# Optimization experiments

Hardware: AMD Instinct MI355X
Metric: run time of the kernel (lower is better)

The kernel has to match this reference:

```python
import jax, jax.numpy as jnp
import numpy as np

EPS = 1e-5

def bn_eval(x, p):
    # p: [4, C] = gamma, beta, running_mean, running_var; channel-last broadcast
    g, b, m, v = p[0], p[1], p[2], p[3]
    return (x - m) * (g / jnp.sqrt(v + EPS)) + b

def _bn_params(k, c):
    k1, k2, k3, k4 = jax.random.split(k, 4)
    gamma = jax.random.uniform(k1, (c,)) + 0.5
    beta = jax.random.normal(k2, (c,)) * 0.1
    mean = jax.random.normal(k3, (c,)) * 0.1
    var = jax.random.uniform(k4, (c,)) + 0.5
    return jnp.stack([gamma, beta, mean, var])

def _lin(k, fan_in, fan_out):
    bound = 1.0 / np.sqrt(fan_in)
    kw, kb = jax.random.split(k)
    w = jax.random.uniform(kw, (fan_in, fan_out), minval=-bound, maxval=bound)
    b = jax.random.uniform(kb, (fan_out,), minval=-bound, maxval=bound)
    return w, b

def setup_inputs() -> dict:
    key = jax.random.key(0)
    B, N, S, C, G = 2, 4096, 16, 256, 8
    ks = jax.random.split(key, 20)
    feats = jax.random.normal(ks[0], (B, N, C), dtype=jnp.float32)
    coords = jax.random.normal(ks[1], (B, N, 3), dtype=jnp.float32)
    index = jax.random.randint(ks[2], (B, N, S), 0, N, dtype=jnp.int32)
    wq, bq = _lin(ks[3], C, C); bnq = _bn_params(ks[4], C)
    wk, bk = _lin(ks[5], C, C); bnk = _bn_params(ks[6], C)
    wv, bv = _lin(ks[7], C, C)
    pm_w1, pm_b1 = _lin(ks[8], 3, C); pm_bn = _bn_params(ks[9], C)
    pm_w2, pm_b2 = _lin(ks[10], C, C)
    pb_w1, pb_b1 = _lin(ks[11], 3, C); pb_bn = _bn_params(ks[12], C)
    pb_w2, pb_b2 = _lin(ks[13], C, C)
    we_w1, we_b1 = _lin(ks[14], C, G); we_bn = _bn_params(ks[15], G)
    we_w2, we_b2 = _lin(ks[16], G, G)
    return dict(feats=feats, coords=coords, index=index,
                wq=wq, bq=bq, bnq=bnq, wk=wk, bk=bk, bnk=bnk, wv=wv, bv=bv,
                pm_w1=pm_w1, pm_b1=pm_b1, pm_bn=pm_bn, pm_w2=pm_w2, pm_b2=pm_b2,
                pb_w1=pb_w1, pb_b1=pb_b1, pb_bn=pb_bn, pb_w2=pb_w2, pb_b2=pb_b2,
                we_w1=we_w1, we_b1=we_b1, we_bn=we_bn, we_w2=we_w2, we_b2=we_b2)

def reference(feats, coords, index,
              wq, bq, bnq, wk, bk, bnk, wv, bv,
              pm_w1, pm_b1, pm_bn, pm_w2, pm_b2,
              pb_w1, pb_b1, pb_bn, pb_w2, pb_b2,
              we_w1, we_b1, we_bn, we_w2, we_b2):
    B, N, C = feats.shape
    S = index.shape[2]
    G = we_w1.shape[1]
    q = jax.nn.relu(bn_eval(feats @ wq + bq, bnq))                       # [B,N,C]
    k = jax.nn.relu(bn_eval(feats @ wk + bk, bnk))                       # [B,N,C]
    v = feats @ wv + bv                                                   # [B,N,C]
    idx = index.reshape(B, N * S)
    key_g = jnp.take_along_axis(k, idx[:, :, None], axis=1).reshape(B, N, S, C)
    val_g = jnp.take_along_axis(v, idx[:, :, None], axis=1).reshape(B, N, S, C)
    crd_g = jnp.take_along_axis(coords, idx[:, :, None], axis=1).reshape(B, N, S, 3)
    relation_qk = key_g - q[:, :, None, :]                                # [B,N,S,C]
    pos = coords[:, :, None, :] - crd_g                                   # [B,N,S,3]
    pem = jax.nn.relu(bn_eval(pos @ pm_w1 + pm_b1, pm_bn)) @ pm_w2 + pm_b2
    relation_qk = relation_qk * pem
    peb = jax.nn.relu(bn_eval(pos @ pb_w1 + pb_b1, pb_bn)) @ pb_w2 + pb_b2
    relation_qk = relation_qk + peb
    val_g = val_g + peb
    w = jax.nn.relu(bn_eval(relation_qk @ we_w1 + we_b1, we_bn)) @ we_w2 + we_b2  # [B,N,S,G]
    w = jax.nn.softmax(w, axis=2)                                         # softmax over neighbors
    val_g = val_g.reshape(B, N, S, G, C // G)
    out = jnp.einsum('bnsgi,bnsg->bngi', val_g, w).reshape(B, N, C)
    return out
```

## Files before the change

### kernel.cpp

```cpp
#include <hip/hip_runtime.h>
#include <hip/hip_bf16.h>


typedef __attribute__((ext_vector_type(8))) short bf16x8_t;
typedef __attribute__((ext_vector_type(4))) float f32x4_t;
typedef __attribute__((ext_vector_type(2))) float v2f;

#define BN_EPS 1e-5f
#define WSYNC() asm volatile("s_waitcnt lgkmcnt(0)" ::: "memory")

__device__ __forceinline__ float blo(unsigned int v) {
    union { unsigned int u; float f; } x; x.u = v << 16; return x.f;
}
__device__ __forceinline__ float bhi(unsigned int v) {
    union { unsigned int u; float f; } x; x.u = v & 0xffff0000u; return x.f;
}
__device__ __forceinline__ v2f upk(unsigned int v) {
    v2f r; r.x = blo(v); r.y = bhi(v); return r;
}
__device__ __forceinline__ unsigned int fbits(float f) {
    union { float f; unsigned int u; } x; x.f = f; return x.u;
}
__device__ __forceinline__ unsigned short f2b(float f) {
    unsigned int u = fbits(f);
    return (unsigned short)((u + 0x7fffu + ((u >> 16) & 1u)) >> 16);
}
__device__ __forceinline__ unsigned int f2bpk(float a, float b) {
    union { __hip_bfloat162 h; unsigned int u; } x;
    x.h = __float22bfloat162_rn(make_float2(a, b));
    return x.u;
}
__device__ __forceinline__ unsigned int f2bpk2(v2f v) { return f2bpk(v.x, v.y); }
__device__ __forceinline__ unsigned int relpair(unsigned int kb, unsigned int qb,
                                                unsigned int pm_, unsigned int pb_) {
    v2f d = upk(kb) - upk(qb);
    v2f r = __builtin_elementwise_fma(d, upk(pm_), upk(pb_));
    return f2bpk2(r);
}

__global__ __launch_bounds__(256) void k_prep(
    const float* __restrict__ wq, const float* __restrict__ wk,
    const float* __restrict__ wv, const float* __restrict__ pm2,
    const float* __restrict__ pb2,
    const float* __restrict__ pm_w1, const float* __restrict__ pm_b1,
    const float* __restrict__ pm_bn,
    const float* __restrict__ pb_w1, const float* __restrict__ pb_b1,
    const float* __restrict__ pb_bn,
    const float* __restrict__ we_w1,
    unsigned short* __restrict__ wsT, float* __restrict__ W4,
    unsigned short* __restrict__ we1TF)
{
    const int bid = blockIdx.x, t = threadIdx.x;
    if (bid < 160) {
        __shared__ unsigned short T[32][72];
        const int mat = bid >> 5;
        const int kk  = (bid >> 2) & 7;
        const int ntq = bid & 3;
        const float* s = (mat == 0) ? wq : (mat == 1) ? wk : (mat == 2) ? wv
                         : (mat == 3) ? pm2 : pb2;
        {
            int c = t & 63, r0 = t >> 6;
            for (int i = 0; i < 8; ++i) {
                int r = r0 + i * 4;
                T[r][c] = f2b(s[(kk * 32 + r) * 256 + ntq * 64 + c]);
            }
        }
        __syncthreads();
        {
            int seg = t >> 6, lane = t & 63;
            int col = seg * 16 + (lane & 15);
            int kr  = (lane >> 4) * 8;
            unsigned int v[8];
            #pragma unroll
            for (int j = 0; j < 8; ++j) v[j] = T[kr + j][col];
            uint4 o;
            o.x = v[0] | (v[1] << 16);
            o.y = v[2] | (v[3] << 16);
            o.z = v[4] | (v[5] << 16);
            o.w = v[6] | (v[7] << 16);
            *(uint4*)(wsT + mat * 65536 + (ntq * 4 + seg) * 4096 + kk * 512 + lane * 8) = o;
        }
    } else if (bid == 160) {
        int c = t;
        float s = pm_bn[c] / sqrtf(pm_bn[768 + c] + BN_EPS);
        float4 wm = make_float4(pm_w1[c] * s, pm_w1[256 + c] * s, pm_w1[512 + c] * s,
                                (pm_b1[c] - pm_bn[512 + c]) * s + pm_bn[256 + c]);
        s = pb_bn[c] / sqrtf(pb_bn[768 + c] + BN_EPS);
        float4 wb = make_float4(pb_w1[c] * s, pb_w1[256 + c] * s, pb_w1[512 + c] * s,
                                (pb_b1[c] - pb_bn[512 + c]) * s + pb_bn[256 + c]);
        ((float4*)W4)[c]       = wm;
        ((float4*)W4)[256 + c] = wb;
    } else {
        for (int j = 0; j < 8; ++j) {
            int e = t * 8 + j;
            int g = e >> 8, c = e & 255;
            we1TF[g * 256 + c] = f2b(we_w1[c * 8 + g]);
        }
    }
}

__global__ __launch_bounds__(256) void k_qkv(
    const float* __restrict__ feats,
    const unsigned short* __restrict__ wT,
    const float* __restrict__ bq, const float* __restrict__ bnq,
    const float* __restrict__ bk, const float* __restrict__ bnk,
    const float* __restrict__ bv,
    unsigned short* __restrict__ qkv)
{
    __shared__ unsigned short A[32][264];
    const int t    = threadIdx.x;
    const int widx = blockIdx.x >> 8;
    const int mb   = blockIdx.x & 255;

    for (int i = 0; i < 8; ++i) {
        int row = 4 * i + (t >> 6), col = (t & 63) * 4;
        float4 f = *(const float4*)(feats + (mb * 32 + row) * 256 + col);
        *(uint2*)&A[row][col] = make_uint2(f2bpk(f.x, f.y), f2bpk(f.z, f.w));
    }
    __syncthreads();

    const int lane = t & 63, w = t >> 6;
    const int ln15 = lane & 15, quad = lane >> 4;
    const int mt = w & 1, nh = w >> 1;

    bf16x8_t afr[8];
    #pragma unroll
    for (int kk = 0; kk < 8; ++kk)
        afr[kk] = *(const bf16x8_t*)&A[mt * 16 + ln15][kk * 32 + quad * 8];

    const unsigned short* W = wT + widx * 65536;
    const float* bias = (widx == 0) ? bq : (widx == 1) ? bk : bv;
    const float* bn   = (widx == 0) ? bnq : (widx == 1) ? bnk : nullptr;
    unsigned short* dst = qkv + (size_t)widx * 8192 * 256;

    f32x4_t acc[8];
    for (int j = 0; j < 8; ++j) acc[j] = (f32x4_t){0.f, 0.f, 0.f, 0.f};

    #pragma unroll
    for (int kk = 0; kk < 8; ++kk) {
        #pragma unroll
        for (int j = 0; j < 8; ++j) {
            int nt = nh * 8 + j;
            bf16x8_t bfr = *(const bf16x8_t*)(W + ((nt * 8 + kk) * 64 + lane) * 8);
            acc[j] = __builtin_amdgcn_mfma_f32_16x16x32_bf16(afr[kk], bfr, acc[j], 0, 0, 0);
        }
    }

    float bb[8], sc[8], mu[8], be[8];
    #pragma unroll
    for (int j = 0; j < 8; ++j) {
        int c = (nh * 8 + j) * 16 + ln15;
        bb[j] = bias[c];
        if (bn) {
            sc[j] = bn[c] / sqrtf(bn[768 + c] + BN_EPS);
            be[j] = bn[256 + c];
            mu[j] = bn[512 + c];
        }
    }
    __syncthreads();
    #pragma unroll
    for (int j = 0; j < 8; ++j) {
        int c = (nh * 8 + j) * 16 + ln15;
        float y[4];
        for (int r = 0; r < 4; ++r) {
            y[r] = acc[j][r] + bb[j];
            if (bn) y[r] = fmaxf((y[r] - mu[j]) * sc[j] + be[j], 0.f);
        }
        for (int r = 0; r < 4; r += 2) {
            unsigned int pk = f2bpk(y[r], y[r + 1]);
            A[mt * 16 + quad * 4 + r][c]     = (unsigned short)pk;
            A[mt * 16 + quad * 4 + r + 1][c] = (unsigned short)(pk >> 16);
        }
    }
    __syncthreads();
    {
        int row = t >> 3, cc = (t & 7) * 32;
        #pragma unroll
        for (int j = 0; j < 4; ++j) {
            uint4 v = *(const uint4*)&A[row][cc + 8 * j];
            *(uint4*)(dst + (mb * 32 + row) * 256 + cc + 8 * j) = v;
        }
    }
}

__global__ __launch_bounds__(512, 4) void k_main(
    const float* __restrict__ coords,
    const int*   __restrict__ index,
    const unsigned short* __restrict__ qm,
    const unsigned short* __restrict__ km,
    const unsigned short* __restrict__ vm,
    const unsigned short* __restrict__ pmw2F,
    const unsigned short* __restrict__ pbw2F,
    const float* __restrict__ W4,
    const unsigned short* __restrict__ we1TF,
    const float* __restrict__ pm_b2, const float* __restrict__ pb_b2,
    const float* __restrict__ we_b1, const float* __restrict__ we_bn,
    const float* __restrict__ we_w2, const float* __restrict__ we_b2,
    float* __restrict__ out)
{
    __shared__ unsigned short bufR[64][264];
    __shared__ unsigned short bufP[64][264];
    __shared__ float posA[64][4];
    __shared__ float usP[2][64][8];
    __shared__ float us_[64][8];
    __shared__ int   rowg_[64];
    __shared__ float we2s[8][8];
    __shared__ float web2[8], swe8[8], dwe8[8];

    const int t   = threadIdx.x;
    const int P0  = blockIdx.x * 4;
    const int bb_ = P0 >> 12;
    const int w = t >> 6, lane = t & 63;
    const int ln15 = lane & 15, quad = lane >> 4;
    const int p   = w >> 1, sub = w & 1;
    const int R0  = p * 16;
    const int Pg  = P0 + p;

    const int rg = (bb_ << 12) + index[Pg * 16 + ln15];
    uint4 kpre[4];
    #pragma unroll
    for (int kk = 0; kk < 4; ++kk)
        kpre[kk] = *(const uint4*)(km + rg * 256 + (sub * 4 + kk) * 32 + quad * 8);

    if (lane < 8) {
        int m  = w * 8 + lane;
        int Pr = P0 + (m >> 4);
        int rs = (bb_ << 12) + index[Pr * 16 + (m & 15)];
        rowg_[m]   = rs;
        posA[m][0] = coords[Pr * 3 + 0] - coords[rs * 3 + 0];
        posA[m][1] = coords[Pr * 3 + 1] - coords[rs * 3 + 1];
        posA[m][2] = coords[Pr * 3 + 2] - coords[rs * 3 + 2];
        posA[m][3] = 0.f;
    }
    if (t < 64) we2s[t >> 3][t & 7] = we_w2[t];
    if (t < 8) {
        float s = we_bn[t] / sqrtf(we_bn[24 + t] + BN_EPS);
        swe8[t] = s;
        dwe8[t] = (we_b1[t] - we_bn[16 + t]) * s + we_bn[8 + t];
        web2[t] = we_b2[t];
    }
    WSYNC();

    const int hc = lane * 4;
    const int hm = w * 8;

    v2f w0a, w1a, w2a, w3a, w0b, w1b, w2b, w3b;
    v2f x0a, x1a, x2a, x3a, x0b, x1b, x2b, x3b;
    {
        float4 A0 = ((const float4*)W4)[hc],     A1 = ((const float4*)W4)[hc + 1];
        float4 A2 = ((const float4*)W4)[hc + 2], A3 = ((const float4*)W4)[hc + 3];
        w0a = (v2f){A0.x, A1.x}; w1a = (v2f){A0.y, A1.y};
        w2a = (v2f){A0.z, A1.z}; w3a = (v2f){A0.w, A1.w};
        w0b = (v2f){A2.x, A3.x}; w1b = (v2f){A2.y, A3.y};
        w2b = (v2f){A2.z, A3.z}; w3b = (v2f){A2.w, A3.w};
        float4 B0 = ((const float4*)W4)[256 + hc],     B1 = ((const float4*)W4)[256 + hc + 1];
        float4 B2 = ((const float4*)W4)[256 + hc + 2], B3 = ((const float4*)W4)[256 + hc + 3];
        x0a = (v2f){B0.x, B1.x}; x1a = (v2f){B0.y, B1.y};
        x2a = (v2f){B0.z, B1.z}; x3a = (v2f){B0.w, B1.w};
        x0b = (v2f){B2.x, B3.x}; x1b = (v2f){B2.y, B3.y};
        x2b = (v2f){B2.z, B3.z}; x3b = (v2f){B2.w, B3.w};
    }
    const v2f vz = {0.f, 0.f};

    #pragma unroll
    for (int m = 0; m < 8; ++m) {
        float4 pp = *(const float4*)&posA[hm + m][0];
        v2f px = (v2f){pp.x, pp.x}, py = (v2f){pp.y, pp.y}, pz = (v2f){pp.z, pp.z};
        v2f ha = __builtin_elementwise_fma(px, x0a,
                 __builtin_elementwise_fma(py, x1a,
                 __builtin_elementwise_fma(pz, x2a, x3a)));
        v2f hb = __builtin_elementwise_fma(px, x0b,
                 __builtin_elementwise_fma(py, x1b,
                 __builtin_elementwise_fma(pz, x2b, x3b)));
        ha = __builtin_elementwise_max(ha, vz);
        hb = __builtin_elementwise_max(hb, vz);
        *(uint2*)&bufR[hm + m][hc] = make_uint2(f2bpk2(ha), f2bpk2(hb));
    }
    __syncthreads();

    f32x4_t acc[2][4];
    {
        float b0 = pb_b2[(w * 2    ) * 16 + ln15];
        float b1 = pb_b2[(w * 2 + 1) * 16 + ln15];
        for (int mt = 0; mt < 4; ++mt) {
            acc[0][mt] = (f32x4_t){b0, b0, b0, b0};
            acc[1][mt] = (f32x4_t){b1, b1, b1, b1};
        }
    }
    #pragma unroll
    for (int kk = 0; kk < 8; ++kk) {
        bf16x8_t afr[4];
        #pragma unroll
        for (int mt = 0; mt < 4; ++mt)
            afr[mt] = *(const bf16x8_t*)&bufR[mt * 16 + ln15][kk * 32 + quad * 8];
        #pragma unroll
        for (int ntl = 0; ntl < 2; ++ntl) {
            int nt = w * 2 + ntl;
            bf16x8_t bfr = *(const bf16x8_t*)(pbw2F + ((nt * 8 + kk) * 64 + lane) * 8);
            #pragma unroll
            for (int mt = 0; mt < 4; ++mt)
                acc[ntl][mt] = __builtin_amdgcn_mfma_f32_16x16x32_bf16(afr[mt], bfr, acc[ntl][mt], 0, 0, 0);
        }
    }
    __syncthreads();

    #pragma unroll
    for (int ntl = 0; ntl < 2; ++ntl) {
        int c = (w * 2 + ntl) * 16 + ln15;
        for (int mt = 0; mt < 4; ++mt)
            for (int r = 0; r < 4; r += 2) {
                unsigned int pk = f2bpk(acc[ntl][mt][r], acc[ntl][mt][r + 1]);
                bufP[mt * 16 + quad * 4 + r][c]     = (unsigned short)pk;
                bufP[mt * 16 + quad * 4 + r + 1][c] = (unsigned short)(pk >> 16);
            }
    }
    #pragma unroll
    for (int m = 0; m < 8; ++m) {
        float4 pp = *(const float4*)&posA[hm + m][0];
        v2f px = (v2f){pp.x, pp.x}, py = (v2f){pp.y, pp.y}, pz = (v2f){pp.z, pp.z};
        v2f ha = __builtin_elementwise_fma(px, w0a,
                 __builtin_elementwise_fma(py, w1a,
                 __builtin_elementwise_fma(pz, w2a, w3a)));
        v2f hb = __builtin_elementwise_fma(px, w0b,
                 __builtin_elementwise_fma(py, w1b,
                 __builtin_elementwise_fma(pz, w2b, w3b)));
        ha = __builtin_elementwise_max(ha, vz);
        hb = __builtin_elementwise_max(hb, vz);
        *(uint2*)&bufR[hm + m][hc] = make_uint2(f2bpk2(ha), f2bpk2(hb));
    }
    __syncthreads();

    {
        float b0 = pm_b2[(w * 2    ) * 16 + ln15];
        float b1 = pm_b2[(w * 2 + 1) * 16 + ln15];
        for (int mt = 0; mt < 4; ++mt) {
            acc[0][mt] = (f32x4_t){b0, b0, b0, b0};
            acc[1][mt] = (f32x4_t){b1, b1, b1, b1};
        }
    }
    #pragma unroll
    for (int kk = 0; kk < 8; ++kk) {
        bf16x8_t afr[4];
        #pragma unroll
        for (int mt = 0; mt < 4; ++mt)
            afr[mt] = *(const bf16x8_t*)&bufR[mt * 16 + ln15][kk * 32 + quad * 8];
        #pragma unroll
        for (int ntl = 0; ntl < 2; ++ntl) {
            int nt = w * 2 + ntl;
            bf16x8_t bfr = *(const bf16x8_t*)(pmw2F + ((nt * 8 + kk) * 64 + lane) * 8);
            #pragma unroll
            for (int mt = 0; mt < 4; ++mt)
                acc[ntl][mt] = __builtin_amdgcn_mfma_f32_16x16x32_bf16(afr[mt], bfr, acc[ntl][mt], 0, 0, 0);
        }
    }
    __syncthreads();

    #pragma unroll
    for (int ntl = 0; ntl < 2; ++ntl) {
        int c = (w * 2 + ntl) * 16 + ln15;
        for (int mt = 0; mt < 4; ++mt)
            for (int r = 0; r < 4; r += 2) {
                unsigned int pk = f2bpk(acc[ntl][mt][r], acc[ntl][mt][r + 1]);
                bufR[mt * 16 + quad * 4 + r][c]     = (unsigned short)pk;
                bufR[mt * 16 + quad * 4 + r + 1][c] = (unsigned short)(pk >> 16);
            }
    }
    __syncthreads();

    {
        const bf16x8_t bz = {0, 0, 0, 0, 0, 0, 0, 0};
        f32x4_t lacc = {0.f, 0.f, 0.f, 0.f};
        #pragma unroll
        for (int kk = 0; kk < 4; ++kk) {
            int cb8 = (sub * 4 + kk) * 32 + quad * 8;
            uint4 pm4 = *(const uint4*)&bufR[R0 + ln15][cb8];
            uint4 pb4 = *(const uint4*)&bufP[R0 + ln15][cb8];
            uint4 q4  = *(const uint4*)(qm + Pg * 256 + cb8);
            union { uint4 u; bf16x8_t v; } rr;
            rr.u.x = relpair(kpre[kk].x, q4.x, pm4.x, pb4.x);
            rr.u.y = relpair(kpre[kk].y, q4.y, pm4.y, pb4.y);
            rr.u.z = relpair(kpre[kk].z, q4.z, pm4.z, pb4.z);
            rr.u.w = relpair(kpre[kk].w, q4.w, pm4.w, pb4.w);
            bf16x8_t bfr = bz;
            if (ln15 < 8) bfr = *(const bf16x8_t*)(we1TF + ln15 * 256 + cb8);
            lacc = __builtin_amdgcn_mfma_f32_16x16x32_bf16(rr.v, bfr, lacc, 0, 0, 0);
        }
        if (ln15 < 8) {
            #pragma unroll
            for (int r = 0; r < 4; ++r)
                usP[sub][R0 + quad * 4 + r][ln15] = lacc[r];
        }
    }
    __syncthreads();

    if (sub == 0 && lane < 16) {
        int s = lane;
        float uv[8], l[8];
        #pragma unroll
        for (int g = 0; g < 8; ++g) {
            float x = usP[0][R0 + s][g] + usP[1][R0 + s][g];
            uv[g] = fmaxf(x * swe8[g] + dwe8[g], 0.f);
        }
        #pragma unroll
        for (int g = 0; g < 8; ++g) {
            float x = web2[g];
            for (int gp = 0; gp < 8; ++gp) x += uv[gp] * we2s[gp][g];
            l[g] = x;
        }
        #pragma unroll
        for (int g = 0; g < 8; ++g) us_[R0 + s][g] = l[g];
    }
    WSYNC();

    if (sub == 0 && lane < 8) {
        int g = lane;
        float mx = -1e30f;
        for (int s = 0; s < 16; ++s) mx = fmaxf(mx, us_[R0 + s][g]);
        float e[16], sum = 0.f;
        for (int s = 0; s < 16; ++s) { e[s] = __expf(us_[R0 + s][g] - mx); sum += e[s]; }
        float inv = 1.f / sum;
        for (int s = 0; s < 16; ++s) us_[R0 + s][g] = e[s] * inv;
    }
    __syncthreads();

    {
        int idx2 = sub * 64 + lane;
        int c5 = idx2 * 2, g = c5 >> 5;
        v2f a = {0.f, 0.f};
        #pragma unroll
        for (int s = 0; s < 16; ++s) {
            int rv = rowg_[R0 + s];
            float wv_ = us_[R0 + s][g];
            unsigned int v2 = *(const unsigned int*)(vm + rv * 256 + c5);
            unsigned int p2 = *(const unsigned int*)&bufP[R0 + s][c5];
            v2f ws = (v2f){wv_, wv_};
            a = __builtin_elementwise_fma(ws, upk(v2) + upk(p2), a);
        }
        *(float2*)(out + (size_t)Pg * 256 + c5) = make_float2(a.x, a.y);
    }
}

extern "C" void kernel_launch(void* const* d_in, const int* in_sizes, int n_in,
                              void* d_out, int out_size, void* d_ws, size_t ws_size,
                              hipStream_t stream)
{
    const float* feats  = (const float*)d_in[0];
    const float* coords = (const float*)d_in[1];
    const int*   index  = (const int*)d_in[2];
    const float* wq     = (const float*)d_in[3];
    const float* bq     = (const float*)d_in[4];
    const float* bnq    = (const float*)d_in[5];
    const float* wk     = (const float*)d_in[6];
    const float* bk     = (const float*)d_in[7];
    const float* bnk    = (const float*)d_in[8];
    const float* wv     = (const float*)d_in[9];
    const float* bv     = (const float*)d_in[10];
    const float* pm_w1  = (const float*)d_in[11];
    const float* pm_b1  = (const float*)d_in[12];
    const float* pm_bn  = (const float*)d_in[13];
    const float* pm_w2  = (const float*)d_in[14];
    const float* pm_b2  = (const float*)d_in[15];
    const float* pb_w1  = (const float*)d_in[16];
    const float* pb_b1  = (const float*)d_in[17];
    const float* pb_bn  = (const float*)d_in[18];
    const float* pb_w2  = (const float*)d_in[19];
    const float* pb_b2  = (const float*)d_in[20];
    const float* we_w1  = (const float*)d_in[21];
    const float* we_b1  = (const float*)d_in[22];
    const float* we_bn  = (const float*)d_in[23];
    const float* we_w2  = (const float*)d_in[24];
    const float* we_b2  = (const float*)d_in[25];

    unsigned short* qkv   = (unsigned short*)d_ws;
    unsigned short* wsT   = qkv + (size_t)3 * 8192 * 256;
    float*          W4    = (float*)(wsT + 5 * 65536);
    unsigned short* we1TF = (unsigned short*)(W4 + 2048);

    const size_t need = (size_t)13238272 + 8192 + 4096;
    if (ws_size < need) {
        hipMemsetAsync(d_out, 0, (size_t)out_size * 4, stream);
        return;
    }

    k_prep<<<162,  256, 0, stream>>>(wq, wk, wv, pm_w2, pb_w2,
                                     pm_w1, pm_b1, pm_bn,
                                     pb_w1, pb_b1, pb_bn,
                                     we_w1, wsT, W4, we1TF);
    k_qkv <<<768,  256, 0, stream>>>(feats, wsT, bq, bnq, bk, bnk, bv, qkv);
    k_main<<<2048, 512, 0, stream>>>(coords, index,
                                     qkv,
                                     qkv + (size_t)8192 * 256,
                                     qkv + (size_t)2 * 8192 * 256,
                                     wsT + 3 * 65536,
                                     wsT + 4 * 65536,
                                     W4, we1TF,
                                     pm_b2, pb_b2,
                                     we_b1, we_bn, we_w2, we_b2,
                                     (float*)d_out);
}
```

Baseline: 199.3 us.

## Run pos-bias and pos-mult GEMMs concurrently across wave halves, prefetch q

Both positional hidden layers are computed up front into separate LDS buffers. The eight waves then split into two halves, one running the pb GEMM and the other the pm GEMM, each wave covering four N-tiles. Each half writes its result into the other's buffer. This removes one serial GEMM phase and two block barriers. The q row is also prefetched from global memory alongside the gathered key, instead of being loaded inside the relation loop. The cost is that each wave now holds 16 accumulator tiles instead of 8, which raises register pressure and may lower occupancy.

```diff
diff --git a/kernel.cpp b/kernel.cpp
--- a/kernel.cpp
+++ b/kernel.cpp
@@ -215,12 +215,17 @@
     const int p   = w >> 1, sub = w & 1;
     const int R0  = p * 16;
     const int Pg  = P0 + p;
+    const int half = w >> 2;
+    const int wq4  = w & 3;
 
     const int rg = (bb_ << 12) + index[Pg * 16 + ln15];
-    uint4 kpre[4];
-    #pragma unroll
-    for (int kk = 0; kk < 4; ++kk)
-        kpre[kk] = *(const uint4*)(km + rg * 256 + (sub * 4 + kk) * 32 + quad * 8);
+    uint4 kpre[4], qpre[4];
+    #pragma unroll
+    for (int kk = 0; kk < 4; ++kk) {
+        int off = (sub * 4 + kk) * 32 + quad * 8;
+        kpre[kk] = *(const uint4*)(km + rg * 256 + off);
+        qpre[kk] = *(const uint4*)(qm + Pg * 256 + off);
+    }
 
     if (lane < 8) {
         int m  = w * 8 + lane;
@@ -243,60 +248,75 @@
 
     const int hc = lane * 4;
     const int hm = w * 8;
-
-    v2f w0a, w1a, w2a, w3a, w0b, w1b, w2b, w3b;
-    v2f x0a, x1a, x2a, x3a, x0b, x1b, x2b, x3b;
+    const v2f vz = {0.f, 0.f};
+
+    {
+        float4 B0 = ((const float4*)W4)[256 + hc],     B1 = ((const float4*)W4)[256 + hc + 1];
+        float4 B2 = ((const float4*)W4)[256 + hc + 2], B3 = ((const float4*)W4)[256 + hc + 3];
+        v2f x0a = (v2f){B0.x, B1.x}, x1a = (v2f){B0.y, B1.y};
+        v2f x2a = (v2f){B0.z, B1.z}, x3a = (v2f){B0.w, B1.w};
+        v2f x0b = (v2f){B2.x, B3.x}, x1b = (v2f){B2.y, B3.y};
+        v2f x2b = (v2f){B2.z, B3.z}, x3b = (v2f){B2.w, B3.w};
+        #pragma unroll
+        for (int m = 0; m < 8; ++m) {
+            float4 pp = *(const float4*)&posA[hm + m][0];
+            v2f px = (v2f){pp.x, pp.x}, py = (v2f){pp.y, pp.y}, pz = (v2f){pp.z, pp.z};
+            v2f ha = __builtin_elementwise_fma(px, x0a,
+                     __builtin_elementwise_fma(py, x1a,
+                     __builtin_elementwise_fma(pz, x2a, x3a)));
+            v2f hb = __builtin_elementwise_fma(px, x0b,
+                     __builtin_elementwise_fma(py, x1b,
+                     __builtin_elementwise_fma(pz, x2b, x3b)));
+            ha = __builtin_elementwise_max(ha, vz);
+            hb = __builtin_elementwise_max(hb, vz);
+            *(uint2*)&bufR[hm + m][hc] = make_uint2(f2bpk2(ha), f2bpk2(hb));
+        }
+    }
     {
         float4 A0 = ((const float4*)W4)[hc],     A1 = ((const float4*)W4)[hc + 1];
         float4 A2 = ((const float4*)W4)[hc + 2], A3 = ((const float4*)W4)[hc + 3];
-        w0a = (v2f){A0.x, A1.x}; w1a = (v2f){A0.y, A1.y};
-        w2a = (v2f){A0.z, A1.z}; w3a = (v2f){A0.w, A1.w};
-        w0b = (v2f){A2.x, A3.x}; w1b = (v2f){A2.y, A3.y};
-        w2b = (v2f){A2.z, A3.z}; w3b = (v2f){A2.w, A3.w};
-        float4 B0 = ((const float4*)W4)[256 + hc],     B1 = ((const float4*)W4)[256 + hc + 1];
-        float4 B2 = ((const float4*)W4)[256 + hc + 2], B3 = ((const float4*)W4)[256 + hc + 3];
-        x0a = (v2f){B0.x, B1.x}; x1a = (v2f){B0.y, B1.y};
-        x2a = (v2f){B0.z, B1.z}; x3a = (v2f){B0.w, B1.w};
-        x0b = (v2f){B2.x, B3.x}; x1b = (v2f){B2.y, B3.y};
-        x2b = (v2f){B2.z, B3.z}; x3b = (v2f){B2.w, B3.w};
-    }
-    const v2f vz = {0.f, 0.f};
-
-    #pragma unroll
-    for (int m = 0; m < 8; ++m) {
-        float4 pp = *(const float4*)&posA[hm + m][0];
-        v2f px = (v2f){pp.x, pp.x}, py = (v2f){pp.y, pp.y}, pz = (v2f){pp.z, pp.z};
-        v2f ha = __builtin_elementwise_fma(px, x0a,
-                 __builtin_elementwise_fma(py, x1a,
-                 __builtin_elementwise_fma(pz, x2a, x3a)));
-        v2f hb = __builtin_elementwise_fma(px, x0b,
-                 __builtin_elementwise_fma(py, x1b,
-                 __builtin_elementwise_fma(pz, x2b, x3b)));
-        ha = __builtin_elementwise_max(ha, vz);
-        hb = __builtin_elementwise_max(hb, vz);
-        *(uint2*)&bufR[hm + m][hc] = make_uint2(f2bpk2(ha), f2bpk2(hb));
-    }
-    __syncthreads();
-
-    f32x4_t acc[2][4];
-    {
-        float b0 = pb_b2[(w * 2    ) * 16 + ln15];
-        float b1 = pb_b2[(w * 2 + 1) * 16 + ln15];
-        for (int mt = 0; mt < 4; ++mt) {
-            acc[0][mt] = (f32x4_t){b0, b0, b0, b0};
-            acc[1][mt] = (f32x4_t){b1, b1, b1, b1};
-        }
+        v2f w0a = (v2f){A0.x, A1.x}, w1a = (v2f){A0.y, A1.y};
+        v2f w2a = (v2f){A0.z, A1.z}, w3a = (v2f){A0.w, A1.w};
+        v2f w0b = (v2f){A2.x, A3.x}, w1b = (v2f){A2.y, A3.y};
+        v2f w2b = (v2f){A2.z, A3.z}, w3b = (v2f){A2.w, A3.w};
+        #pragma unroll
+        for (int m = 0; m < 8; ++m) {
+            float4 pp = *(const float4*)&posA[hm + m][0];
+            v2f px = (v2f){pp.x, pp.x}, py = (v2f){pp.y, pp.y}, pz = (v2f){pp.z, pp.z};
+            v2f ha = __builtin_elementwise_fma(px, w0a,
+                     __builtin_elementwise_fma(py, w1a,
+                     __builtin_elementwise_fma(pz, w2a, w3a)));
+            v2f hb = __builtin_elementwise_fma(px, w0b,
+                     __builtin_elementwise_fma(py, w1b,
+                     __builtin_elementwise_fma(pz, w2b, w3b)));
+            ha = __builtin_elementwise_max(ha, vz);
+            hb = __builtin_elementwise_max(hb, vz);
+            *(uint2*)&bufP[hm + m][hc] = make_uint2(f2bpk2(ha), f2bpk2(hb));
+        }
+    }
+    __syncthreads();
+
+    const unsigned short* Wf = half ? pmw2F : pbw2F;
+    const float* b2 = half ? pm_b2 : pb_b2;
+    const unsigned short (*hbuf)[264] = half ? (const unsigned short (*)[264])bufP
+                                             : (const unsigned short (*)[264])bufR;
+    f32x4_t acc[4][4];
+    #pragma unroll
+    for (int ntl = 0; ntl < 4; ++ntl) {
+        float bv_ = b2[(wq4 * 4 + ntl) * 16 + ln15];
+        for (int mt = 0; mt < 4; ++mt)
+            acc[ntl][mt] = (f32x4_t){bv_, bv_, bv_, bv_};
     }
     #pragma unroll
     for (int kk = 0; kk < 8; ++kk) {
         bf16x8_t afr[4];
         #pragma unroll
         for (int mt = 0; mt < 4; ++mt)
-            afr[mt] = *(const bf16x8_t*)&bufR[mt * 16 + ln15][kk * 32 + quad * 8];
-        #pragma unroll
-        for (int ntl = 0; ntl < 2; ++ntl) {
-            int nt = w * 2 + ntl;
-            bf16x8_t bfr = *(const bf16x8_t*)(pbw2F + ((nt * 8 + kk) * 64 + lane) * 8);
+            afr[mt] = *(const bf16x8_t*)&hbuf[mt * 16 + ln15][kk * 32 + quad * 8];
+        #pragma unroll
+        for (int ntl = 0; ntl < 4; ++ntl) {
+            int nt = wq4 * 4 + ntl;
+            bf16x8_t bfr = *(const bf16x8_t*)(Wf + ((nt * 8 + kk) * 64 + lane) * 8);
             #pragma unroll
             for (int mt = 0; mt < 4; ++mt)
                 acc[ntl][mt] = __builtin_amdgcn_mfma_f32_16x16x32_bf16(afr[mt], bfr, acc[ntl][mt], 0, 0, 0);
@@ -304,66 +324,18 @@
     }
     __syncthreads();
 
-    #pragma unroll
-    for (int ntl = 0; ntl < 2; ++ntl) {
-        int c = (w * 2 + ntl) * 16 + ln15;
-        for (int mt = 0; mt < 4; ++mt)
-            for (int r = 0; r < 4; r += 2) {
-                unsigned int pk = f2bpk(acc[ntl][mt][r], acc[ntl][mt][r + 1]);
-                bufP[mt * 16 + quad * 4 + r][c]     = (unsigned short)pk;
-                bufP[mt * 16 + quad * 4 + r + 1][c] = (unsigned short)(pk >> 16);
-            }
-    }
-    #pragma unroll
-    for (int m = 0; m < 8; ++m) {
-        float4 pp = *(const float4*)&posA[hm + m][0];
-        v2f px = (v2f){pp.x, pp.x}, py = (v2f){pp.y, pp.y}, pz = (v2f){pp.z, pp.z};
-        v2f ha = __builtin_elementwise_fma(px, w0a,
-                 __builtin_elementwise_fma(py, w1a,
-                 __builtin_elementwise_fma(pz, w2a, w3a)));
-        v2f hb = __builtin_elementwise_fma(px, w0b,
-                 __builtin_elementwise_fma(py, w1b,
-                 __builtin_elementwise_fma(pz, w2b, w3b)));
-        ha = __builtin_elementwise_max(ha, vz);
-        hb = __builtin_elementwise_max(hb, vz);
-        *(uint2*)&bufR[hm + m][hc] = make_uint2(f2bpk2(ha), f2bpk2(hb));
-    }
-    __syncthreads();
-
-    {
-        float b0 = pm_b2[(w * 2    ) * 16 + ln15];
-        float b1 = pm_b2[(w * 2 + 1) * 16 + ln15];
-        for (int mt = 0; mt < 4; ++mt) {
-            acc[0][mt] = (f32x4_t){b0, b0, b0, b0};
-            acc[1][mt] = (f32x4_t){b1, b1, b1, b1};
-        }
-    }
-    #pragma unroll
-    for (int kk = 0; kk < 8; ++kk) {
-        bf16x8_t afr[4];
-        #pragma unroll
-        for (int mt = 0; mt < 4; ++mt)
-            afr[mt] = *(const bf16x8_t*)&bufR[mt * 16 + ln15][kk * 32 + quad * 8];
-        #pragma unroll
-        for (int ntl = 0; ntl < 2; ++ntl) {
-            int nt = w * 2 + ntl;
-            bf16x8_t bfr = *(const bf16x8_t*)(pmw2F + ((nt * 8 + kk) * 64 + lane) * 8);
-            #pragma unroll
+    {
+        unsigned short (*obuf)[264] = half ? bufR : bufP;
+        #pragma unroll
+        for (int ntl = 0; ntl < 4; ++ntl) {
+            int c = (wq4 * 4 + ntl) * 16 + ln15;
             for (int mt = 0; mt < 4; ++mt)
-                acc[ntl][mt] = __builtin_amdgcn_mfma_f32_16x16x32_bf16(afr[mt], bfr, acc[ntl][mt], 0, 0, 0);
-        }
-    }
-    __syncthreads();
-
-    #pragma unroll
-    for (int ntl = 0; ntl < 2; ++ntl) {
-        int c = (w * 2 + ntl) * 16 + ln15;
-        for (int mt = 0; mt < 4; ++mt)
-            for (int r = 0; r < 4; r += 2) {
-                unsigned int pk = f2bpk(acc[ntl][mt][r], acc[ntl][mt][r + 1]);
-                bufR[mt * 16 + quad * 4 + r][c]     = (unsigned short)pk;
-                bufR[mt * 16 + quad * 4 + r + 1][c] = (unsigned short)(pk >> 16);
-            }
+                for (int r = 0; r < 4; r += 2) {
+                    unsigned int pk = f2bpk(acc[ntl][mt][r], acc[ntl][mt][r + 1]);
+                    obuf[mt * 16 + quad * 4 + r][c]     = (unsigned short)pk;
+                    obuf[mt * 16 + quad * 4 + r + 1][c] = (unsigned short)(pk >> 16);
+                }
+        }
     }
     __syncthreads();
 
@@ -375,12 +347,11 @@
             int cb8 = (sub * 4 + kk) * 32 + quad * 8;
             uint4 pm4 = *(const uint4*)&bufR[R0 + ln15][cb8];
             uint4 pb4 = *(const uint4*)&bufP[R0 + ln15][cb8];
-            uint4 q4  = *(const uint4*)(qm + Pg * 256 + cb8);
             union { uint4 u; bf16x8_t v; } rr;
-            rr.u.x = relpair(kpre[kk].x, q4.x, pm4.x, pb4.x);
-            rr.u.y = relpair(kpre[kk].y, q4.y, pm4.y, pb4.y);
-            rr.u.z = relpair(kpre[kk].z, q4.z, pm4.z, pb4.z);
-            rr.u.w = relpair(kpre[kk].w, q4.w, pm4.w, pb4.w);
+            rr.u.x = relpair(kpre[kk].x, qpre[kk].x, pm4.x, pb4.x);
+            rr.u.y = relpair(kpre[kk].y, qpre[kk].y, pm4.y, pb4.y);
+            rr.u.z = relpair(kpre[kk].z, qpre[kk].z, pm4.z, pb4.z);
+            rr.u.w = relpair(kpre[kk].w, qpre[kk].w, pm4.w, pb4.w);
             bf16x8_t bfr = bz;
             if (ln15 < 8) bfr = *(const bf16x8_t*)(we1TF + ln15 * 256 + cb8);
             lacc = __builtin_amdgcn_mfma_f32_16x16x32_bf16(rr.v, bfr, lacc, 0, 0, 0);
```

After: 230.7 us. 15.7% more time.
